# Kernel optimization log

Measured on AMD Instinct MI355X. Metric: run time of the kernel, lower is better.

Reference implementation:

```python
import jax, jax.numpy as jnp
import numpy as np

NUM_CLASSES = 80
NUM_TOP_QUERIES = 300


def setup_inputs() -> dict:
    key = jax.random.key(0)
    k1, k2, k3 = jax.random.split(key, 3)
    N, Q, K = 256, 1000, NUM_CLASSES
    logits = jax.random.normal(k1, (N, Q, K), dtype=jnp.float32)
    boxes = jax.random.uniform(k2, (N, Q, 4), dtype=jnp.float32)  # cxcywh in [0,1]
    original_sizes = jax.random.randint(k3, (N, 2), 1, 1280, dtype=jnp.int32)  # (h, w)
    return {"logits": logits, "boxes": boxes, "original_sizes": original_sizes}


def reference(logits, boxes, original_sizes):
    # cxcywh -> xywh (top-left x,y plus w,h)
    cxcy, wh = boxes[..., :2], boxes[..., 2:]
    boxes_xy = jnp.concatenate([cxcy - wh * 0.5, wh], axis=-1)  # (N, Q, 4)
    # torch code uses only original_sizes[0], flipped (h,w)->(w,h), tiled to (w,h,w,h)
    sizes_wh = jnp.tile(original_sizes[0][::-1].astype(boxes.dtype), 2)  # (4,)
    boxes_xy = boxes_xy * sizes_wh
    # sigmoid scores, flatten class dim into query dim, top-k over Q*K
    N = logits.shape[0]
    scores_flat = jax.nn.sigmoid(logits).reshape(N, -1)  # (N, Q*K)
    scores, index = jax.lax.top_k(scores_flat, NUM_TOP_QUERIES)  # (N, 300)
    labels = index % NUM_CLASSES
    qidx = index // NUM_CLASSES
    # gather selected boxes per batch row
    sel_boxes = jax.vmap(lambda b, i: b[i])(boxes_xy, qidx)  # (N, 300, 4)
    out = jnp.concatenate(
        [labels[..., None].astype(scores.dtype), scores[..., None], sel_boxes], axis=-1
    )  # (N, 300, 6): (class_id, confidence, x, y, w, h)
    return out
```

## Files before the change

kernel.cpp:

```cpp
#include <hip/hip_runtime.h>
#include <stdint.h>


#define TOPK 300
#define NCLS 80
#define NQ 1000
#define QK (NQ * NCLS)
#define NB 2048
#define CAP 2048
#define THREADS 1024
#define LAST_VALID 544
#define T0F 2.4f

typedef unsigned long long u64;

__device__ __forceinline__ uint32_t ordf(float f) {
  uint32_t u = __float_as_uint(f);
  return (u & 0x80000000u) ? ~u : (u | 0x80000000u);
}
__device__ __forceinline__ float unordf(uint32_t o) {
  uint32_t u = (o & 0x80000000u) ? (o & 0x7fffffffu) : ~o;
  return __uint_as_float(u);
}

__global__ __launch_bounds__(THREADS) void detr_post_kernel(
    const float* __restrict__ logits, const float* __restrict__ boxes,
    const int* __restrict__ osz, float* __restrict__ out) {
  __shared__ uint32_t hist4[NB * 4];
  __shared__ uint32_t histf[NB];
  __shared__ u64 buf[CAP];
  __shared__ uint32_t sh_sel[3];
  __shared__ uint32_t sh_cnt;

  const int n = blockIdx.x;
  const int t = threadIdx.x;
  const float* lg = logits + (size_t)n * QK;

  if (t == 0) sh_cnt = 0;
  __syncthreads();

#pragma unroll 5
  for (int j = 0; j < 19; ++j) {
    const int i = 4 * t + 4096 * j;
    const float4 v = *(const float4*)(lg + i);
    if (v.x >= T0F) {
      const uint32_t p = atomicAdd(&sh_cnt, 1u);
      if (p < CAP) buf[p] = ((u64)ordf(v.x) << 32) | (u64)(~(uint32_t)(i + 0));
    }
    if (v.y >= T0F) {
      const uint32_t p = atomicAdd(&sh_cnt, 1u);
      if (p < CAP) buf[p] = ((u64)ordf(v.y) << 32) | (u64)(~(uint32_t)(i + 1));
    }
    if (v.z >= T0F) {
      const uint32_t p = atomicAdd(&sh_cnt, 1u);
      if (p < CAP) buf[p] = ((u64)ordf(v.z) << 32) | (u64)(~(uint32_t)(i + 2));
    }
    if (v.w >= T0F) {
      const uint32_t p = atomicAdd(&sh_cnt, 1u);
      if (p < CAP) buf[p] = ((u64)ordf(v.w) << 32) | (u64)(~(uint32_t)(i + 3));
    }
  }
  if (t < LAST_VALID) {
    const int i = 4 * t + 4096 * 19;
    const float4 v = *(const float4*)(lg + i);
    if (v.x >= T0F) {
      const uint32_t p = atomicAdd(&sh_cnt, 1u);
      if (p < CAP) buf[p] = ((u64)ordf(v.x) << 32) | (u64)(~(uint32_t)(i + 0));
    }
    if (v.y >= T0F) {
      const uint32_t p = atomicAdd(&sh_cnt, 1u);
      if (p < CAP) buf[p] = ((u64)ordf(v.y) << 32) | (u64)(~(uint32_t)(i + 1));
    }
    if (v.z >= T0F) {
      const uint32_t p = atomicAdd(&sh_cnt, 1u);
      if (p < CAP) buf[p] = ((u64)ordf(v.z) << 32) | (u64)(~(uint32_t)(i + 2));
    }
    if (v.w >= T0F) {
      const uint32_t p = atomicAdd(&sh_cnt, 1u);
      if (p < CAP) buf[p] = ((u64)ordf(v.w) << 32) | (u64)(~(uint32_t)(i + 3));
    }
  }
  __syncthreads();

  uint32_t cnt = sh_cnt;
  const bool fast_ok = (cnt >= TOPK && cnt <= CAP);

  if (!fast_ok) {
    uint32_t T = 0, S_above = 0, Krem = TOPK;
    int prev_shift = 32;
    const uint32_t sub = (uint32_t)(t & 3);
    const int shifts[3] = {21, 10, 0};
    const int nbns[3] = {2048, 2048, 1024};

    for (int lvl = 0; lvl < 3; ++lvl) {
      const int sh = shifts[lvl];
      const uint32_t nb = (uint32_t)nbns[lvl];

      for (int b = t; b < NB * 4; b += THREADS) hist4[b] = 0;
      __syncthreads();
      for (int j = 0; j < 20; ++j) {
        if (j == 19 && t >= LAST_VALID) break;
        const int i = 4 * t + 4096 * j;
        const float4 v = *(const float4*)(lg + i);
        const float vs[4] = {v.x, v.y, v.z, v.w};
        for (int c = 0; c < 4; ++c) {
          const uint32_t u = ordf(vs[c]);
          if (lvl == 0 || (u >> prev_shift) == (T >> prev_shift))
            atomicAdd(&hist4[(((u >> sh) & (nb - 1)) << 2) | sub], 1u);
        }
      }
      __syncthreads();

      for (uint32_t b = t; b < nb; b += (uint32_t)THREADS) {
        const uint32_t i4 = b << 2;
        histf[b] = hist4[i4] + hist4[i4 + 1] + hist4[i4 + 2] + hist4[i4 + 3];
      }
      __syncthreads();

      for (uint32_t off = 1; off < nb; off <<= 1) {
        uint32_t a0 = histf[t] + ((t + off < nb) ? histf[t + off] : 0u);
        uint32_t a1 = 0;
        if (nb > (uint32_t)THREADS) {
          const uint32_t i1 = (uint32_t)t + THREADS;
          a1 = histf[i1] + ((i1 + off < nb) ? histf[i1 + off] : 0u);
        }
        __syncthreads();
        histf[t] = a0;
        if (nb > (uint32_t)THREADS) histf[(uint32_t)t + THREADS] = a1;
        __syncthreads();
      }

      for (uint32_t b = t; b < nb; b += (uint32_t)THREADS) {
        const uint32_t s = histf[b];
        const uint32_t sn = (b + 1 < nb) ? histf[b + 1] : 0u;
        if (s >= Krem && sn < Krem) {
          sh_sel[0] = b;
          sh_sel[1] = sn;
          sh_sel[2] = s;
        }
      }
      __syncthreads();
      const uint32_t bsel = sh_sel[0], above = sh_sel[1], candL = sh_sel[2];
      __syncthreads();

      T |= bsel << sh;
      if (S_above + candL <= CAP || lvl == 2) break;
      S_above += above;
      Krem -= above;
      prev_shift = sh;
    }

    if (t == 0) sh_cnt = 0;
    __syncthreads();
    for (int j = 0; j < 20; ++j) {
      if (j == 19 && t >= LAST_VALID) break;
      const int i = 4 * t + 4096 * j;
      const float4 v = *(const float4*)(lg + i);
      const float vs[4] = {v.x, v.y, v.z, v.w};
      for (int c = 0; c < 4; ++c) {
        const uint32_t u = ordf(vs[c]);
        if (u >= T) {
          const uint32_t p = atomicAdd(&sh_cnt, 1u);
          if (p < CAP) buf[p] = ((u64)u << 32) | (u64)(~(uint32_t)(i + c));
        }
      }
    }
    __syncthreads();
    cnt = sh_cnt < CAP ? sh_cnt : CAP;
  }

  const uint32_t cnt4 = (cnt + 3u) & ~3u;
  for (uint32_t p = cnt + t; p < cnt4; p += (uint32_t)THREADS) buf[p] = 0ULL;
  __syncthreads();

  const float s0 = (float)osz[0];
  const float s1 = (float)osz[1];
  for (uint32_t p = t; p < cnt; p += (uint32_t)THREADS) {
    const u64 my = buf[p];
    uint32_t rank = 0;
    for (uint32_t q = 0; q < cnt4; q += 4) {
      const u64 k0 = buf[q + 0], k1 = buf[q + 1];
      const u64 k2 = buf[q + 2], k3 = buf[q + 3];
      rank += (uint32_t)(k0 > my) + (uint32_t)(k1 > my) +
              (uint32_t)(k2 > my) + (uint32_t)(k3 > my);
    }
    if (rank < TOPK) {
      const uint32_t u = (uint32_t)(my >> 32);
      const uint32_t idx = ~(uint32_t)(my & 0xffffffffu);
      const float lgv = unordf(u);
      const float score = 1.0f / (1.0f + expf(-lgv));
      const uint32_t q = idx / NCLS;
      const uint32_t lab = idx - q * NCLS;
      const float* bp = boxes + ((size_t)n * NQ + q) * 4;
      const float cx = bp[0], cy = bp[1], w = bp[2], h = bp[3];
      float* op = out + ((size_t)n * TOPK + rank) * 6;
      op[0] = (float)lab;
      op[1] = score;
      op[2] = (cx - 0.5f * w) * s1;
      op[3] = (cy - 0.5f * h) * s0;
      op[4] = w * s1;
      op[5] = h * s0;
    }
  }
}

extern "C" void kernel_launch(void* const* d_in, const int* in_sizes, int n_in,
                              void* d_out, int out_size, void* d_ws, size_t ws_size,
                              hipStream_t stream) {
  const float* logits = (const float*)d_in[0];
  const float* boxes = (const float*)d_in[1];
  const int* osz = (const int*)d_in[2];
  float* out = (float*)d_out;
  const int nbatch = in_sizes[0] / QK;
  detr_post_kernel<<<nbatch, THREADS, 0, stream>>>(logits, boxes, osz, out);
}
```

Measured before the change: 133.1 us.

## Replace O(n^2) rank counting with histogram bucket sort and intra-bucket ranking

The all-pairs rank computation over the candidate buffer is replaced with a counting sort. Candidates are bucketed by their ordered-float key above a base threshold into a 2048-bin histogram, and a prefix scan turns the counts into bucket offsets. Each candidate is scattered into its bucket and then ranked only against the entries in its own bucket. This removes the quadratic shared-memory scan, at the cost of extra histogram, scan and scatter phases with several more block barriers. Shared memory is reorganised so the histogram space is aliased with the new buffers.

Result: faster. 124.7 us (-6.3%).

```diff
diff --git a/kernel.cpp b/kernel.cpp
--- a/kernel.cpp
+++ b/kernel.cpp
@@ -11,6 +11,7 @@
 #define THREADS 1024
 #define LAST_VALID 544
 #define T0F 2.4f
+#define RSH 12
 
 typedef unsigned long long u64;
 
@@ -26,11 +27,16 @@
 __global__ __launch_bounds__(THREADS) void detr_post_kernel(
     const float* __restrict__ logits, const float* __restrict__ boxes,
     const int* __restrict__ osz, float* __restrict__ out) {
-  __shared__ uint32_t hist4[NB * 4];
+  __shared__ u64 buf[CAP];
+  __shared__ u64 smem64[4096];
   __shared__ uint32_t histf[NB];
-  __shared__ u64 buf[CAP];
   __shared__ uint32_t sh_sel[3];
   __shared__ uint32_t sh_cnt;
+
+  uint32_t* const hist4 = (uint32_t*)smem64;
+  u64* const buf2 = smem64;
+  uint32_t* const rh = (uint32_t*)(smem64 + 2048);
+  uint32_t* const rcur = (uint32_t*)(smem64 + 3072);
 
   const int n = blockIdx.x;
   const int t = threadIdx.x;
@@ -84,6 +90,7 @@
 
   uint32_t cnt = sh_cnt;
   const bool fast_ok = (cnt >= TOPK && cnt <= CAP);
+  uint32_t baseord = ordf(T0F);
 
   if (!fast_ok) {
     uint32_t T = 0, S_above = 0, Krem = TOPK;
@@ -167,26 +174,63 @@
     }
     __syncthreads();
     cnt = sh_cnt < CAP ? sh_cnt : CAP;
-  }
-
-  const uint32_t cnt4 = (cnt + 3u) & ~3u;
-  for (uint32_t p = cnt + t; p < cnt4; p += (uint32_t)THREADS) buf[p] = 0ULL;
+    baseord = T;
+  }
+
+  for (int b = t; b < NB; b += THREADS) rh[b] = 0;
+  __syncthreads();
+
+  const u64 k0 = ((uint32_t)t < cnt) ? buf[t] : 0ULL;
+  const u64 k1 = ((uint32_t)(t + THREADS) < cnt) ? buf[t + THREADS] : 0ULL;
+  uint32_t b0 = 0, b1 = 0;
+  if ((uint32_t)t < cnt) {
+    b0 = ((uint32_t)(k0 >> 32) - baseord) >> RSH;
+    if (b0 > NB - 1u) b0 = NB - 1u;
+    atomicAdd(&rh[b0], 1u);
+  }
+  if ((uint32_t)(t + THREADS) < cnt) {
+    b1 = ((uint32_t)(k1 >> 32) - baseord) >> RSH;
+    if (b1 > NB - 1u) b1 = NB - 1u;
+    atomicAdd(&rh[b1], 1u);
+  }
+  __syncthreads();
+
+  for (int b = t; b < NB; b += THREADS) rcur[b] = rh[b];
+  __syncthreads();
+  for (uint32_t off = 1; off < NB; off <<= 1) {
+    const uint32_t i1 = (uint32_t)t + THREADS;
+    const uint32_t a0 =
+        rcur[t] + (((uint32_t)t + off < NB) ? rcur[t + off] : 0u);
+    const uint32_t a1 = rcur[i1] + ((i1 + off < NB) ? rcur[i1 + off] : 0u);
+    __syncthreads();
+    rcur[t] = a0;
+    rcur[i1] = a1;
+    __syncthreads();
+  }
+  for (int b = t; b < NB; b += THREADS) rcur[b] -= rh[b];
+  __syncthreads();
+
+  if ((uint32_t)t < cnt) {
+    const uint32_t s = atomicAdd(&rcur[b0], 1u);
+    buf2[s] = k0;
+  }
+  if ((uint32_t)(t + THREADS) < cnt) {
+    const uint32_t s = atomicAdd(&rcur[b1], 1u);
+    buf2[s] = k1;
+  }
   __syncthreads();
 
   const float s0 = (float)osz[0];
   const float s1 = (float)osz[1];
-  for (uint32_t p = t; p < cnt; p += (uint32_t)THREADS) {
-    const u64 my = buf[p];
-    uint32_t rank = 0;
-    for (uint32_t q = 0; q < cnt4; q += 4) {
-      const u64 k0 = buf[q + 0], k1 = buf[q + 1];
-      const u64 k2 = buf[q + 2], k3 = buf[q + 3];
-      rank += (uint32_t)(k0 > my) + (uint32_t)(k1 > my) +
-              (uint32_t)(k2 > my) + (uint32_t)(k3 > my);
-    }
+
+  if ((uint32_t)t < cnt) {
+    const uint32_t end = rcur[b0];
+    const uint32_t beg = end - rh[b0];
+    uint32_t rank = beg;
+    for (uint32_t q = beg; q < end; ++q) rank += (uint32_t)(buf2[q] > k0);
     if (rank < TOPK) {
-      const uint32_t u = (uint32_t)(my >> 32);
-      const uint32_t idx = ~(uint32_t)(my & 0xffffffffu);
+      const uint32_t u = (uint32_t)(k0 >> 32);
+      const uint32_t idx = ~(uint32_t)(k0 & 0xffffffffu);
       const float lgv = unordf(u);
       const float score = 1.0f / (1.0f + expf(-lgv));
       const uint32_t q = idx / NCLS;
@@ -202,6 +246,29 @@
       op[5] = h * s0;
     }
   }
+  if ((uint32_t)(t + THREADS) < cnt) {
+    const uint32_t end = rcur[b1];
+    const uint32_t beg = end - rh[b1];
+    uint32_t rank = beg;
+    for (uint32_t q = beg; q < end; ++q) rank += (uint32_t)(buf2[q] > k1);
+    if (rank < TOPK) {
+      const uint32_t u = (uint32_t)(k1 >> 32);
+      const uint32_t idx = ~(uint32_t)(k1 & 0xffffffffu);
+      const float lgv = unordf(u);
+      const float score = 1.0f / (1.0f + expf(-lgv));
+      const uint32_t q = idx / NCLS;
+      const uint32_t lab = idx - q * NCLS;
+      const float* bp = boxes + ((size_t)n * NQ + q) * 4;
+      const float cx = bp[0], cy = bp[1], w = bp[2], h = bp[3];
+      float* op = out + ((size_t)n * TOPK + rank) * 6;
+      op[0] = (float)lab;
+      op[1] = score;
+      op[2] = (cx - 0.5f * w) * s1;
+      op[3] = (cy - 0.5f * h) * s0;
+      op[4] = w * s1;
+      op[5] = h * s0;
+    }
+  }
 }
 
 extern "C" void kernel_launch(void* const* d_in, const int* in_sizes, int n_in,
```

## Replace all-pairs rank counting with bucketed counting sort plus in-bin ranking

Applied to the files above, without the earlier changes.

The all-pairs rank computation over up to 2048 candidates is replaced. The kernel now builds a 512-bin histogram of candidate keys above the threshold, takes a wave-level descending prefix scan to get bin offsets, scatters the keys into bin order, and ranks each key by counting only the larger keys in its own bin. This cuts the O(cnt^2) shared-memory comparisons to roughly O(cnt × bin size), at the cost of extra atomics, barriers and a scan. The histogram scratch is aliased onto the existing shared buffer, and box loads and output stores are vectorised.

After: 124.4 us. -6.5%, faster.

```diff
diff --git a/kernel.cpp b/kernel.cpp
--- a/kernel.cpp
+++ b/kernel.cpp
@@ -11,6 +11,8 @@
 #define THREADS 1024
 #define LAST_VALID 544
 #define T0F 2.4f
+#define RNB 512
+#define RSH 14
 
 typedef unsigned long long u64;
 
@@ -23,20 +25,50 @@
   return __uint_as_float(u);
 }
 
+__device__ __forceinline__ void rank_emit(
+    const u64 key, const uint32_t bin, const uint32_t* rcur,
+    const uint32_t* rh, const u64* buf2, const float* boxes, float* out,
+    const int n, const float s0, const float s1) {
+  const uint32_t end = rcur[bin];
+  const uint32_t beg = end - rh[bin];
+  uint32_t rank = beg;
+  for (uint32_t q = beg; q < end; ++q) rank += (uint32_t)(buf2[q] > key);
+  if (rank < TOPK) {
+    const uint32_t u = (uint32_t)(key >> 32);
+    const uint32_t idx = ~(uint32_t)(key & 0xffffffffu);
+    const float lgv = unordf(u);
+    const float score = 1.0f / (1.0f + expf(-lgv));
+    const uint32_t q = idx / NCLS;
+    const uint32_t lab = idx - q * NCLS;
+    const float4 b4 = *(const float4*)(boxes + ((size_t)n * NQ + q) * 4);
+    float* op = out + ((size_t)n * TOPK + rank) * 6;
+    float2* op2 = (float2*)op;
+    op2[0] = make_float2((float)lab, score);
+    op2[1] = make_float2((b4.x - 0.5f * b4.z) * s1, (b4.y - 0.5f * b4.w) * s0);
+    op2[2] = make_float2(b4.z * s1, b4.w * s0);
+  }
+}
+
 __global__ __launch_bounds__(THREADS) void detr_post_kernel(
     const float* __restrict__ logits, const float* __restrict__ boxes,
     const int* __restrict__ osz, float* __restrict__ out) {
-  __shared__ uint32_t hist4[NB * 4];
+  __shared__ u64 buf[CAP];
+  __shared__ u64 smem64[4096];
   __shared__ uint32_t histf[NB];
-  __shared__ u64 buf[CAP];
   __shared__ uint32_t sh_sel[3];
   __shared__ uint32_t sh_cnt;
+
+  uint32_t* const hist4 = (uint32_t*)smem64;
+  u64* const buf2 = smem64;
+  uint32_t* const rh = (uint32_t*)(smem64 + 2048);
+  uint32_t* const rcur = (uint32_t*)(smem64 + 2304);
 
   const int n = blockIdx.x;
   const int t = threadIdx.x;
   const float* lg = logits + (size_t)n * QK;
 
   if (t == 0) sh_cnt = 0;
+  if (t < RNB) rh[t] = 0;
   __syncthreads();
 
 #pragma unroll 5
@@ -84,6 +116,7 @@
 
   uint32_t cnt = sh_cnt;
   const bool fast_ok = (cnt >= TOPK && cnt <= CAP);
+  uint32_t baseord = ordf(T0F);
 
   if (!fast_ok) {
     uint32_t T = 0, S_above = 0, Krem = TOPK;
@@ -152,6 +185,7 @@
 
     if (t == 0) sh_cnt = 0;
     __syncthreads();
+    if (t < RNB) rh[t] = 0;
     for (int j = 0; j < 20; ++j) {
       if (j == 19 && t >= LAST_VALID) break;
       const int i = 4 * t + 4096 * j;
@@ -167,41 +201,64 @@
     }
     __syncthreads();
     cnt = sh_cnt < CAP ? sh_cnt : CAP;
-  }
-
-  const uint32_t cnt4 = (cnt + 3u) & ~3u;
-  for (uint32_t p = cnt + t; p < cnt4; p += (uint32_t)THREADS) buf[p] = 0ULL;
+    baseord = T;
+  }
+
+  const u64 k0 = ((uint32_t)t < cnt) ? buf[t] : 0ULL;
+  const u64 k1 = ((uint32_t)(t + THREADS) < cnt) ? buf[t + THREADS] : 0ULL;
+  uint32_t b0 = 0, b1 = 0;
+  if ((uint32_t)t < cnt) {
+    b0 = ((uint32_t)(k0 >> 32) - baseord) >> RSH;
+    if (b0 > RNB - 1u) b0 = RNB - 1u;
+    atomicAdd(&rh[b0], 1u);
+  }
+  if ((uint32_t)(t + THREADS) < cnt) {
+    b1 = ((uint32_t)(k1 >> 32) - baseord) >> RSH;
+    if (b1 > RNB - 1u) b1 = RNB - 1u;
+    atomicAdd(&rh[b1], 1u);
+  }
+  __syncthreads();
+
+  if (t < 64) {
+    const uint4 a = *(const uint4*)&rh[8 * t];
+    const uint4 b = *(const uint4*)&rh[8 * t + 4];
+    const uint32_t c0 = a.x, c1 = a.y, c2 = a.z, c3 = a.w;
+    const uint32_t c4 = b.x, c5 = b.y, c6 = b.z, c7 = b.w;
+    const uint32_t mysum = c0 + c1 + c2 + c3 + c4 + c5 + c6 + c7;
+    uint32_t s = mysum;
+    for (int d = 1; d < 64; d <<= 1) {
+      const uint32_t o = __shfl_down(s, d);
+      if (t + d < 64) s += o;
+    }
+    uint32_t acc = s - mysum;
+    rcur[8 * t + 7] = acc; acc += c7;
+    rcur[8 * t + 6] = acc; acc += c6;
+    rcur[8 * t + 5] = acc; acc += c5;
+    rcur[8 * t + 4] = acc; acc += c4;
+    rcur[8 * t + 3] = acc; acc += c3;
+    rcur[8 * t + 2] = acc; acc += c2;
+    rcur[8 * t + 1] = acc; acc += c1;
+    rcur[8 * t + 0] = acc;
+  }
+  __syncthreads();
+
+  if ((uint32_t)t < cnt) {
+    const uint32_t s = atomicAdd(&rcur[b0], 1u);
+    buf2[s] = k0;
+  }
+  if ((uint32_t)(t + THREADS) < cnt) {
+    const uint32_t s = atomicAdd(&rcur[b1], 1u);
+    buf2[s] = k1;
+  }
   __syncthreads();
 
   const float s0 = (float)osz[0];
   const float s1 = (float)osz[1];
-  for (uint32_t p = t; p < cnt; p += (uint32_t)THREADS) {
-    const u64 my = buf[p];
-    uint32_t rank = 0;
-    for (uint32_t q = 0; q < cnt4; q += 4) {
-      const u64 k0 = buf[q + 0], k1 = buf[q + 1];
-      const u64 k2 = buf[q + 2], k3 = buf[q + 3];
-      rank += (uint32_t)(k0 > my) + (uint32_t)(k1 > my) +
-              (uint32_t)(k2 > my) + (uint32_t)(k3 > my);
-    }
-    if (rank < TOPK) {
-      const uint32_t u = (uint32_t)(my >> 32);
-      const uint32_t idx = ~(uint32_t)(my & 0xffffffffu);
-      const float lgv = unordf(u);
-      const float score = 1.0f / (1.0f + expf(-lgv));
-      const uint32_t q = idx / NCLS;
-      const uint32_t lab = idx - q * NCLS;
-      const float* bp = boxes + ((size_t)n * NQ + q) * 4;
-      const float cx = bp[0], cy = bp[1], w = bp[2], h = bp[3];
-      float* op = out + ((size_t)n * TOPK + rank) * 6;
-      op[0] = (float)lab;
-      op[1] = score;
-      op[2] = (cx - 0.5f * w) * s1;
-      op[3] = (cy - 0.5f * h) * s0;
-      op[4] = w * s1;
-      op[5] = h * s0;
-    }
-  }
+
+  if ((uint32_t)t < cnt)
+    rank_emit(k0, b0, rcur, rh, buf2, boxes, out, n, s0, s1);
+  if ((uint32_t)(t + THREADS) < cnt)
+    rank_emit(k1, b1, rcur, rh, buf2, boxes, out, n, s0, s1);
 }
 
 extern "C" void kernel_launch(void* const* d_in, const int* in_sizes, int n_in,
```
